# Optimization experiments

Measured on AMD Instinct MI355X. Metric: run time of the kernel, lower is better.

## Reference

```python
import jax, jax.numpy as jnp
import numpy as np

EPS = 1e-8  # matches F.cosine_similarity eps clamp

def _cosine_gram(x):
    # row-normalize with eps clamp, then Gram matrix == pairwise cosine similarity
    norms = jnp.maximum(jnp.linalg.norm(x, axis=-1, keepdims=True), EPS)
    xn = x / norms
    return xn @ xn.T  # [N, N]

def setup_inputs() -> dict:
    key = jax.random.key(0)
    k1, k2 = jax.random.split(key)
    N, D = 4096, 512
    return {
        "cosine_distance_latent": jax.random.normal(k1, (N, D), dtype=jnp.float32),
        "mse_latent": jax.random.normal(k2, (N, D), dtype=jnp.float32),
    }

def reference(cosine_distance_latent, mse_latent):
    # cosine distance matrices: (sim - 1) * -1 == 1 - sim
    cd = 1.0 - _cosine_gram(cosine_distance_latent)  # target
    ed = 1.0 - _cosine_gram(mse_latent)              # predicted
    # KL(softmax(cd) || softmax(ed)) per row, then mean
    log_t = jax.nn.log_softmax(cd, axis=-1)
    log_p = jax.nn.log_softmax(ed, axis=-1)
    t = jnp.exp(log_t)
    kl = jnp.sum(t * (log_t - log_p), axis=-1)
    return jnp.mean(kl)
```

## Files before the change

kernel.cpp:

```cpp
#include <hip/hip_runtime.h>
#include <math.h>

#define NROWS 4096
#define DIM   512
#define BMI   256
#define BNJ   128
#define KSTEPS (DIM / 32)
#define NSLOT (NROWS / BNJ)
#define STB   49152

typedef __bf16 bf16x8 __attribute__((ext_vector_type(8)));
typedef float  f32x4  __attribute__((ext_vector_type(4)));

#define GL16(G, L) __builtin_amdgcn_global_load_lds( \
    (const __attribute__((address_space(1))) void*)(G), \
    (__attribute__((address_space(3))) void*)(L), 16, 0, 0)

__global__ __launch_bounds__(256)
void normalize_kernel(const float* __restrict__ X, const float* __restrict__ Y,
                      __bf16* __restrict__ Xn, __bf16* __restrict__ Yn)
{
    const int wid  = threadIdx.x >> 6;
    const int lane = threadIdx.x & 63;
    const int row  = blockIdx.x * 4 + wid;
    const float* src = blockIdx.y ? Y : X;
    __bf16*      dst = blockIdx.y ? Yn : Xn;

    const float4* s4 = reinterpret_cast<const float4*>(src + (size_t)row * DIM);
    float4 v0 = s4[lane * 2 + 0];
    float4 v1 = s4[lane * 2 + 1];
    float ss = v0.x*v0.x + v0.y*v0.y + v0.z*v0.z + v0.w*v0.w
             + v1.x*v1.x + v1.y*v1.y + v1.z*v1.z + v1.w*v1.w;
    #pragma unroll
    for (int m = 1; m < 64; m <<= 1) ss += __shfl_xor(ss, m);
    const float scale = 1.0f / fmaxf(sqrtf(ss), 1e-8f);

    bf16x8 o;
    o[0] = (__bf16)(v0.x * scale); o[1] = (__bf16)(v0.y * scale);
    o[2] = (__bf16)(v0.z * scale); o[3] = (__bf16)(v0.w * scale);
    o[4] = (__bf16)(v1.x * scale); o[5] = (__bf16)(v1.y * scale);
    o[6] = (__bf16)(v1.z * scale); o[7] = (__bf16)(v1.w * scale);
    *reinterpret_cast<bf16x8*>(dst + (size_t)row * DIM + lane * 8) = o;
}

__global__ __launch_bounds__(512, 2)
void gram_kl_kernel(const __bf16* __restrict__ Xn, const __bf16* __restrict__ Yn,
                    float4* __restrict__ partials)
{
    __shared__ char lds[3 * STB];

    const int tid  = threadIdx.x;
    const int wid  = tid >> 6;
    const int lane = tid & 63;
    const int m  = wid >> 2;
    const int q  = wid & 3;
    const int iq = q & 1;
    const int jq = q >> 1;

    const int g = blockIdx.x;
    const int x = g & 7;
    const int t = g >> 3;
    const int bi = (x & 3) * 4 + (t & 3);
    const int bj = (x >> 2) * 16 + ((t >> 2) & 7) + (t >> 5) * 8;
    const int i0 = bi * BMI;
    const int j0 = bj * BNJ;

    const int xnib = (((tid & 3) ^ ((tid >> 3) & 3)) << 4);
    const size_t so_i0 = ((size_t)(i0 + (tid >> 2)) << 10) + xnib;
    const size_t so_i1 = so_i0 + ((size_t)128 << 10);
    const size_t so_j  = ((size_t)(j0 + (tid >> 2)) << 10) + xnib;
    const int wbase = wid * 1024;

    const char* bx = (const char*)Xn;
    const char* by = (const char*)Yn;

    auto STAGE = [&](int st, int ks) {
        char* base = &lds[st * STB];
        const size_t ko = (size_t)ks << 6;
        GL16(bx + so_i0 + ko, base + 0 * 8192 + wbase);
        GL16(bx + so_i1 + ko, base + 1 * 8192 + wbase);
        GL16(by + so_i0 + ko, base + 2 * 8192 + wbase);
        GL16(by + so_i1 + ko, base + 3 * 8192 + wbase);
        GL16(bx + so_j  + ko, base + 4 * 8192 + wbase);
        GL16(by + so_j  + ko, base + 5 * 8192 + wbase);
    };

    const int rdx = ((lane & 15) << 6) + ((((lane >> 4) ^ ((lane >> 1) & 3))) << 4);
    const int ibase = m * 16384 + iq * 8192;
    const int jbase = 32768 + m * 8192 + jq * 4096;

    f32x4 acc[4][8];
    #pragma unroll
    for (int fj = 0; fj < 4; ++fj)
        #pragma unroll
        for (int fi = 0; fi < 8; ++fi)
            acc[fj][fi] = f32x4{0.f, 0.f, 0.f, 0.f};

    STAGE(0, 0);
    STAGE(1, 1);

    for (int s = 0; s < KSTEPS; ++s) {
        if (s < KSTEPS - 1) asm volatile("s_waitcnt vmcnt(6)" ::: "memory");
        else                asm volatile("s_waitcnt vmcnt(0)" ::: "memory");
        __builtin_amdgcn_s_barrier();
        asm volatile("" ::: "memory");

        const char* base = &lds[(s % 3) * STB];
        bf16x8 aJ[4], bI[8];
        #pragma unroll
        for (int fj = 0; fj < 4; ++fj)
            aJ[fj] = *reinterpret_cast<const bf16x8*>(base + jbase + fj * 1024 + rdx);
        #pragma unroll
        for (int fi = 0; fi < 8; ++fi)
            bI[fi] = *reinterpret_cast<const bf16x8*>(base + ibase + fi * 1024 + rdx);

        if (s + 2 < KSTEPS) STAGE((s + 2) % 3, s + 2);

        #pragma unroll
        for (int fj = 0; fj < 4; ++fj)
            #pragma unroll
            for (int fi = 0; fi < 8; ++fi)
                acc[fj][fi] = __builtin_amdgcn_mfma_f32_16x16x32_bf16(aJ[fj], bI[fi], acc[fj][fi], 0, 0, 0);
    }

    __syncthreads();
    if (m == 1) {
        char* dst = &lds[q * 32768 + lane * 16];
        #pragma unroll
        for (int fj = 0; fj < 4; ++fj)
            #pragma unroll
            for (int fi = 0; fi < 8; ++fi)
                *reinterpret_cast<f32x4*>(dst + (fj * 8 + fi) * 1024) = acc[fj][fi];
    }
    __syncthreads();

    float4 res[8];
    if (m == 0) {
        const char* src = &lds[q * 32768 + lane * 16];
        #pragma unroll
        for (int fi = 0; fi < 8; ++fi) {
            float S = 0.f, U = 0.f, V = 0.f, Q = 0.f;
            #pragma unroll
            for (int fj = 0; fj < 4; ++fj) {
                const f32x4 pb = *reinterpret_cast<const f32x4*>(src + (fj * 8 + fi) * 1024);
                #pragma unroll
                for (int r = 0; r < 4; ++r) {
                    const float a = -acc[fj][fi][r];
                    const float b = -pb[r];
                    const float ea = __expf(a);
                    const float eb = __expf(b);
                    S += ea; U += ea * a; V += ea * b; Q += eb;
                }
            }
            #pragma unroll
            for (int mm = 16; mm <= 32; mm <<= 1) {
                S += __shfl_xor(S, mm);
                U += __shfl_xor(U, mm);
                V += __shfl_xor(V, mm);
                Q += __shfl_xor(Q, mm);
            }
            res[fi] = float4{S, U, V, Q};
        }
        if (jq == 1 && lane < 16) {
            float4* scr = reinterpret_cast<float4*>(&lds[131072]);
            #pragma unroll
            for (int fi = 0; fi < 8; ++fi)
                scr[(iq * 8 + fi) * 16 + lane] = res[fi];
        }
    }
    __syncthreads();
    if (m == 0 && jq == 0 && lane < 16) {
        const float4* scr = reinterpret_cast<const float4*>(&lds[131072]);
        #pragma unroll
        for (int fi = 0; fi < 8; ++fi) {
            const float4 o = scr[(iq * 8 + fi) * 16 + lane];
            const int row = i0 + iq * 128 + fi * 16 + lane;
            partials[(size_t)row * NSLOT + bj] =
                float4{res[fi].x + o.x, res[fi].y + o.y, res[fi].z + o.z, res[fi].w + o.w};
        }
    }
}

__global__ __launch_bounds__(256)
void merge_kernel(const float4* __restrict__ partials, float* __restrict__ blocksum)
{
    __shared__ float w[4];
    const int row = blockIdx.x * 256 + threadIdx.x;
    float S = 0.f, U = 0.f, V = 0.f, Q = 0.f;
    #pragma unroll
    for (int s = 0; s < NSLOT; ++s) {
        const float4 p = partials[(size_t)row * NSLOT + s];
        S += p.x; U += p.y; V += p.z; Q += p.w;
    }
    float kl = (U - V) / S - logf(S) + logf(Q);
    #pragma unroll
    for (int mm = 1; mm < 64; mm <<= 1) kl += __shfl_xor(kl, mm);
    if ((threadIdx.x & 63) == 0) w[threadIdx.x >> 6] = kl;
    __syncthreads();
    if (threadIdx.x == 0) blocksum[blockIdx.x] = w[0] + w[1] + w[2] + w[3];
}

__global__ __launch_bounds__(64)
void reduce_kernel(const float* __restrict__ blocksum, float* __restrict__ out)
{
    float v = (threadIdx.x < 16) ? blocksum[threadIdx.x] : 0.f;
    #pragma unroll
    for (int mm = 1; mm < 16; mm <<= 1) v += __shfl_xor(v, mm);
    if (threadIdx.x == 0) out[0] = v / (float)NROWS;
}

extern "C" void kernel_launch(void* const* d_in, const int* in_sizes, int n_in,
                              void* d_out, int out_size, void* d_ws, size_t ws_size,
                              hipStream_t stream)
{
    const float* X = (const float*)d_in[0];
    const float* Y = (const float*)d_in[1];
    float* out = (float*)d_out;

    char* ws = (char*)d_ws;
    const size_t mat_bytes = (size_t)NROWS * DIM * sizeof(__bf16);
    __bf16* Xn = (__bf16*)ws;
    __bf16* Yn = (__bf16*)(ws + mat_bytes);
    float4* partials = (float4*)(ws + 2 * mat_bytes);
    float* blocksum = (float*)(ws + 2 * mat_bytes + (size_t)NROWS * NSLOT * sizeof(float4));

    normalize_kernel<<<dim3(NROWS / 4, 2), 256, 0, stream>>>(X, Y, Xn, Yn);
    gram_kl_kernel<<<(NROWS / BMI) * (NROWS / BNJ), 512, 0, stream>>>(Xn, Yn, partials);
    merge_kernel<<<NROWS / 256, 256, 0, stream>>>(partials, blocksum);
    reduce_kernel<<<1, 64, 0, stream>>>(blocksum, out);
}
```

Measured before the change: 60.09 us.

## Split GEMM k-step into two phases with sched barriers and MFMA priority

Each k-step of the Gram MFMA loop is split into two half-phases. Half of the I-operand LDS reads are issued, then the global prefetch, and the rest of the I-operand reads overlap with the first 16 MFMAs. Sched barriers fix the instruction order, extra workgroup barriers keep waves in step, and s_setprio raises wave priority during MFMA bursts so waves interleave memory and matrix work. The two extra barriers per k-step add synchronisation cost and may reduce the slack between waves.

```diff
diff --git a/kernel.cpp b/kernel.cpp
--- a/kernel.cpp
+++ b/kernel.cpp
@@ -15,6 +15,8 @@
 #define GL16(G, L) __builtin_amdgcn_global_load_lds( \
     (const __attribute__((address_space(1))) void*)(G), \
     (__attribute__((address_space(3))) void*)(L), 16, 0, 0)
+
+#define SB0() __builtin_amdgcn_sched_barrier(0)
 
 __global__ __launch_bounds__(256)
 void normalize_kernel(const float* __restrict__ X, const float* __restrict__ Y,
@@ -103,24 +105,50 @@
         if (s < KSTEPS - 1) asm volatile("s_waitcnt vmcnt(6)" ::: "memory");
         else                asm volatile("s_waitcnt vmcnt(0)" ::: "memory");
         __builtin_amdgcn_s_barrier();
-        asm volatile("" ::: "memory");
+        SB0();
 
         const char* base = &lds[(s % 3) * STB];
-        bf16x8 aJ[4], bI[8];
+
+        bf16x8 aJ[4], bI0[4], bI1[4];
         #pragma unroll
         for (int fj = 0; fj < 4; ++fj)
             aJ[fj] = *reinterpret_cast<const bf16x8*>(base + jbase + fj * 1024 + rdx);
         #pragma unroll
-        for (int fi = 0; fi < 8; ++fi)
-            bI[fi] = *reinterpret_cast<const bf16x8*>(base + ibase + fi * 1024 + rdx);
-
+        for (int fi = 0; fi < 4; ++fi)
+            bI0[fi] = *reinterpret_cast<const bf16x8*>(base + ibase + fi * 1024 + rdx);
         if (s + 2 < KSTEPS) STAGE((s + 2) % 3, s + 2);
-
-        #pragma unroll
-        for (int fj = 0; fj < 4; ++fj)
-            #pragma unroll
-            for (int fi = 0; fi < 8; ++fi)
-                acc[fj][fi] = __builtin_amdgcn_mfma_f32_16x16x32_bf16(aJ[fj], bI[fi], acc[fj][fi], 0, 0, 0);
+        SB0();
+
+        __builtin_amdgcn_s_barrier();
+        asm volatile("s_waitcnt lgkmcnt(0)" ::: "memory");
+        SB0();
+
+        #pragma unroll
+        for (int fi = 0; fi < 4; ++fi)
+            bI1[fi] = *reinterpret_cast<const bf16x8*>(base + ibase + (4 + fi) * 1024 + rdx);
+        SB0();
+
+        __builtin_amdgcn_s_setprio(1);
+        #pragma unroll
+        for (int fj = 0; fj < 4; ++fj)
+            #pragma unroll
+            for (int fi = 0; fi < 4; ++fi)
+                acc[fj][fi] = __builtin_amdgcn_mfma_f32_16x16x32_bf16(aJ[fj], bI0[fi], acc[fj][fi], 0, 0, 0);
+        __builtin_amdgcn_s_setprio(0);
+        SB0();
+
+        __builtin_amdgcn_s_barrier();
+        asm volatile("s_waitcnt lgkmcnt(0)" ::: "memory");
+        SB0();
+
+        __builtin_amdgcn_s_setprio(1);
+        #pragma unroll
+        for (int fj = 0; fj < 4; ++fj)
+            #pragma unroll
+            for (int fi = 0; fi < 4; ++fi)
+                acc[fj][4 + fi] = __builtin_amdgcn_mfma_f32_16x16x32_bf16(aJ[fj], bI1[fi], acc[fj][4 + fi], 0, 0, 0);
+        __builtin_amdgcn_s_setprio(0);
+        SB0();
     }
 
     __syncthreads();
```

Measured after the change: 64.78 us. 7.8% more time.

## Exploit Gram matrix symmetry by computing only lower-triangular tiles

Applied to the files above, without the earlier changes.

The two Gram matrices are symmetric, so the kernel now computes only the lower-triangular 128x128 tiles. Each off-diagonal tile produces per-row softmax partial sums for both its row block and its transposed column block, written to separate partial slots. This roughly halves the MFMA work and the operand loads. In exchange, tiles shrink to 128x128 with 256 threads, the pipeline drops from triple to double buffering with a full vmcnt(0) wait each step, and the epilogue gains extra shuffle reductions.

```diff
diff --git a/kernel.cpp b/kernel.cpp
--- a/kernel.cpp
+++ b/kernel.cpp
@@ -3,11 +3,11 @@
 
 #define NROWS 4096
 #define DIM   512
-#define BMI   256
-#define BNJ   128
+#define UNIT  128
+#define NP    (NROWS / UNIT)
+#define NTILES (NP * (NP + 1) / 2)
 #define KSTEPS (DIM / 32)
-#define NSLOT (NROWS / BNJ)
-#define STB   49152
+#define NSLOT NP
 
 typedef __bf16 bf16x8 __attribute__((ext_vector_type(8)));
 typedef float  f32x4  __attribute__((ext_vector_type(4)));
@@ -43,140 +43,178 @@
     *reinterpret_cast<bf16x8*>(dst + (size_t)row * DIM + lane * 8) = o;
 }
 
-__global__ __launch_bounds__(512, 2)
+__global__ __launch_bounds__(256, 2)
 void gram_kl_kernel(const __bf16* __restrict__ Xn, const __bf16* __restrict__ Yn,
                     float4* __restrict__ partials)
 {
-    __shared__ char lds[3 * STB];
+    __shared__ char lds[69632];
 
     const int tid  = threadIdx.x;
     const int wid  = tid >> 6;
     const int lane = tid & 63;
-    const int m  = wid >> 2;
-    const int q  = wid & 3;
-    const int iq = q & 1;
-    const int jq = q >> 1;
-
-    const int g = blockIdx.x;
-    const int x = g & 7;
-    const int t = g >> 3;
-    const int bi = (x & 3) * 4 + (t & 3);
-    const int bj = (x >> 2) * 16 + ((t >> 2) & 7) + (t >> 5) * 8;
-    const int i0 = bi * BMI;
-    const int j0 = bj * BNJ;
+    const int m  = wid >> 1;
+    const int iq = wid & 1;
+
+    const int glin = (blockIdx.x & 7) * (NTILES / 8) + (blockIdx.x >> 3);
+    int p = (int)((sqrtf((float)(8 * glin + 1)) - 1.0f) * 0.5f);
+    while ((p + 1) * (p + 2) / 2 <= glin) ++p;
+    while (p * (p + 1) / 2 > glin) --p;
+    const int qcol = glin - p * (p + 1) / 2;
+    const int i0 = p * UNIT;
+    const int j0 = qcol * UNIT;
 
     const int xnib = (((tid & 3) ^ ((tid >> 3) & 3)) << 4);
-    const size_t so_i0 = ((size_t)(i0 + (tid >> 2)) << 10) + xnib;
-    const size_t so_i1 = so_i0 + ((size_t)128 << 10);
-    const size_t so_j  = ((size_t)(j0 + (tid >> 2)) << 10) + xnib;
+    const int r0 = tid >> 2;
+    const size_t so_i = ((size_t)(i0 + r0) << 10) + xnib;
+    const size_t so_j = ((size_t)(j0 + r0) << 10) + xnib;
     const int wbase = wid * 1024;
 
     const char* bx = (const char*)Xn;
     const char* by = (const char*)Yn;
 
     auto STAGE = [&](int st, int ks) {
-        char* base = &lds[st * STB];
+        char* base = &lds[st * 32768];
         const size_t ko = (size_t)ks << 6;
-        GL16(bx + so_i0 + ko, base + 0 * 8192 + wbase);
-        GL16(bx + so_i1 + ko, base + 1 * 8192 + wbase);
-        GL16(by + so_i0 + ko, base + 2 * 8192 + wbase);
-        GL16(by + so_i1 + ko, base + 3 * 8192 + wbase);
-        GL16(bx + so_j  + ko, base + 4 * 8192 + wbase);
-        GL16(by + so_j  + ko, base + 5 * 8192 + wbase);
+        const size_t h = (size_t)64 << 10;
+        GL16(bx + so_i + ko,     base + 0 * 8192 + wbase);
+        GL16(bx + so_i + h + ko, base + 0 * 8192 + 4096 + wbase);
+        GL16(by + so_i + ko,     base + 1 * 8192 + wbase);
+        GL16(by + so_i + h + ko, base + 1 * 8192 + 4096 + wbase);
+        GL16(bx + so_j + ko,     base + 2 * 8192 + wbase);
+        GL16(bx + so_j + h + ko, base + 2 * 8192 + 4096 + wbase);
+        GL16(by + so_j + ko,     base + 3 * 8192 + wbase);
+        GL16(by + so_j + h + ko, base + 3 * 8192 + 4096 + wbase);
     };
 
     const int rdx = ((lane & 15) << 6) + ((((lane >> 4) ^ ((lane >> 1) & 3))) << 4);
-    const int ibase = m * 16384 + iq * 8192;
-    const int jbase = 32768 + m * 8192 + jq * 4096;
-
-    f32x4 acc[4][8];
-    #pragma unroll
-    for (int fj = 0; fj < 4; ++fj)
-        #pragma unroll
-        for (int fi = 0; fi < 8; ++fi)
+    const int ibase = m * 8192 + iq * 4096;
+    const int jbase = 16384 + m * 8192;
+
+    f32x4 acc[8][4];
+    #pragma unroll
+    for (int fj = 0; fj < 8; ++fj)
+        #pragma unroll
+        for (int fi = 0; fi < 4; ++fi)
             acc[fj][fi] = f32x4{0.f, 0.f, 0.f, 0.f};
 
     STAGE(0, 0);
-    STAGE(1, 1);
 
     for (int s = 0; s < KSTEPS; ++s) {
-        if (s < KSTEPS - 1) asm volatile("s_waitcnt vmcnt(6)" ::: "memory");
-        else                asm volatile("s_waitcnt vmcnt(0)" ::: "memory");
+        asm volatile("s_waitcnt vmcnt(0)" ::: "memory");
         __builtin_amdgcn_s_barrier();
         asm volatile("" ::: "memory");
 
-        const char* base = &lds[(s % 3) * STB];
-        bf16x8 aJ[4], bI[8];
-        #pragma unroll
-        for (int fj = 0; fj < 4; ++fj)
+        const char* base = &lds[(s & 1) * 32768];
+        bf16x8 aJ[8], bI[4];
+        #pragma unroll
+        for (int fj = 0; fj < 8; ++fj)
             aJ[fj] = *reinterpret_cast<const bf16x8*>(base + jbase + fj * 1024 + rdx);
         #pragma unroll
-        for (int fi = 0; fi < 8; ++fi)
+        for (int fi = 0; fi < 4; ++fi)
             bI[fi] = *reinterpret_cast<const bf16x8*>(base + ibase + fi * 1024 + rdx);
 
-        if (s + 2 < KSTEPS) STAGE((s + 2) % 3, s + 2);
-
-        #pragma unroll
-        for (int fj = 0; fj < 4; ++fj)
-            #pragma unroll
-            for (int fi = 0; fi < 8; ++fi)
+        if (s + 1 < KSTEPS) STAGE((s + 1) & 1, s + 1);
+
+        #pragma unroll
+        for (int fj = 0; fj < 8; ++fj)
+            #pragma unroll
+            for (int fi = 0; fi < 4; ++fi)
                 acc[fj][fi] = __builtin_amdgcn_mfma_f32_16x16x32_bf16(aJ[fj], bI[fi], acc[fj][fi], 0, 0, 0);
     }
 
     __syncthreads();
     if (m == 1) {
-        char* dst = &lds[q * 32768 + lane * 16];
-        #pragma unroll
-        for (int fj = 0; fj < 4; ++fj)
-            #pragma unroll
-            for (int fi = 0; fi < 8; ++fi)
-                *reinterpret_cast<f32x4*>(dst + (fj * 8 + fi) * 1024) = acc[fj][fi];
-    }
-    __syncthreads();
-
-    float4 res[8];
+        char* dst = &lds[iq * 32768 + lane * 16];
+        #pragma unroll
+        for (int fj = 0; fj < 8; ++fj)
+            #pragma unroll
+            for (int fi = 0; fi < 4; ++fi)
+                *reinterpret_cast<f32x4*>(dst + (fj * 4 + fi) * 1024) = acc[fj][fi];
+    }
+    __syncthreads();
+
+    float* jpart = reinterpret_cast<float*>(&lds[65536]);
+
     if (m == 0) {
-        const char* src = &lds[q * 32768 + lane * 16];
-        #pragma unroll
-        for (int fi = 0; fi < 8; ++fi) {
-            float S = 0.f, U = 0.f, V = 0.f, Q = 0.f;
-            #pragma unroll
-            for (int fj = 0; fj < 4; ++fj) {
-                const f32x4 pb = *reinterpret_cast<const f32x4*>(src + (fj * 8 + fi) * 1024);
+        const char* src = &lds[iq * 32768 + lane * 16];
+        const int sub = lane >> 4;
+        float Si[4] = {0,0,0,0}, Ui[4] = {0,0,0,0}, Vi[4] = {0,0,0,0}, Qi[4] = {0,0,0,0};
+
+        #pragma unroll
+        for (int fj = 0; fj < 8; ++fj) {
+            f32x4 pb[4];
+            #pragma unroll
+            for (int fi = 0; fi < 4; ++fi)
+                pb[fi] = *reinterpret_cast<const f32x4*>(src + (fj * 4 + fi) * 1024);
+
+            float js[4][4];
+            #pragma unroll
+            for (int r = 0; r < 4; ++r) { js[r][0]=0; js[r][1]=0; js[r][2]=0; js[r][3]=0; }
+
+            #pragma unroll
+            for (int fi = 0; fi < 4; ++fi)
                 #pragma unroll
                 for (int r = 0; r < 4; ++r) {
                     const float a = -acc[fj][fi][r];
-                    const float b = -pb[r];
+                    const float b = -pb[fi][r];
                     const float ea = __expf(a);
                     const float eb = __expf(b);
-                    S += ea; U += ea * a; V += ea * b; Q += eb;
+                    Si[fi] += ea; Ui[fi] += ea * a; Vi[fi] += ea * b; Qi[fi] += eb;
+                    js[r][0] += ea; js[r][1] += ea * a; js[r][2] += ea * b; js[r][3] += eb;
+                }
+
+            if (p != qcol) {
+                #pragma unroll
+                for (int r = 0; r < 4; ++r)
+                    #pragma unroll
+                    for (int qq = 0; qq < 4; ++qq) {
+                        #pragma unroll
+                        for (int mk = 1; mk <= 8; mk <<= 1)
+                            js[r][qq] += __shfl_xor(js[r][qq], mk);
+                    }
+                if ((lane & 15) == 0) {
+                    #pragma unroll
+                    for (int r = 0; r < 4; ++r)
+                        #pragma unroll
+                        for (int qq = 0; qq < 4; ++qq)
+                            jpart[(((iq * 4 + sub) * 8 + fj) * 4 + r) * 4 + qq] = js[r][qq];
                 }
             }
-            #pragma unroll
-            for (int mm = 16; mm <= 32; mm <<= 1) {
-                S += __shfl_xor(S, mm);
-                U += __shfl_xor(U, mm);
-                V += __shfl_xor(V, mm);
-                Q += __shfl_xor(Q, mm);
+        }
+
+        #pragma unroll
+        for (int fi = 0; fi < 4; ++fi) {
+            #pragma unroll
+            for (int mk = 16; mk <= 32; mk <<= 1) {
+                Si[fi] += __shfl_xor(Si[fi], mk);
+                Ui[fi] += __shfl_xor(Ui[fi], mk);
+                Vi[fi] += __shfl_xor(Vi[fi], mk);
+                Qi[fi] += __shfl_xor(Qi[fi], mk);
             }
-            res[fi] = float4{S, U, V, Q};
-        }
-        if (jq == 1 && lane < 16) {
-            float4* scr = reinterpret_cast<float4*>(&lds[131072]);
-            #pragma unroll
-            for (int fi = 0; fi < 8; ++fi)
-                scr[(iq * 8 + fi) * 16 + lane] = res[fi];
-        }
-    }
-    __syncthreads();
-    if (m == 0 && jq == 0 && lane < 16) {
-        const float4* scr = reinterpret_cast<const float4*>(&lds[131072]);
-        #pragma unroll
-        for (int fi = 0; fi < 8; ++fi) {
-            const float4 o = scr[(iq * 8 + fi) * 16 + lane];
-            const int row = i0 + iq * 128 + fi * 16 + lane;
-            partials[(size_t)row * NSLOT + bj] =
-                float4{res[fi].x + o.x, res[fi].y + o.y, res[fi].z + o.z, res[fi].w + o.w};
+        }
+        if (lane < 16) {
+            #pragma unroll
+            for (int fi = 0; fi < 4; ++fi) {
+                const int row = i0 + iq * 64 + fi * 16 + lane;
+                partials[(size_t)row * NSLOT + qcol] = float4{Si[fi], Ui[fi], Vi[fi], Qi[fi]};
+            }
+        }
+    }
+    __syncthreads();
+
+    if (p != qcol && wid == 0) {
+        #pragma unroll
+        for (int h = 0; h < 2; ++h) {
+            const int j = h * 64 + lane;
+            const int fj = j >> 4, sub = (j >> 2) & 3, r = j & 3;
+            const int o0 = (((0 * 4 + sub) * 8 + fj) * 4 + r) * 4;
+            const int o1 = (((1 * 4 + sub) * 8 + fj) * 4 + r) * 4;
+            float4 v;
+            v.x = jpart[o0 + 0] + jpart[o1 + 0];
+            v.y = jpart[o0 + 1] + jpart[o1 + 1];
+            v.z = jpart[o0 + 2] + jpart[o1 + 2];
+            v.w = jpart[o0 + 3] + jpart[o1 + 3];
+            partials[(size_t)(j0 + j) * NSLOT + p] = v;
         }
     }
 }
@@ -225,7 +263,7 @@
     float* blocksum = (float*)(ws + 2 * mat_bytes + (size_t)NROWS * NSLOT * sizeof(float4));
 
     normalize_kernel<<<dim3(NROWS / 4, 2), 256, 0, stream>>>(X, Y, Xn, Yn);
-    gram_kl_kernel<<<(NROWS / BMI) * (NROWS / BNJ), 512, 0, stream>>>(Xn, Yn, partials);
+    gram_kl_kernel<<<NTILES, 256, 0, stream>>>(Xn, Yn, partials);
     merge_kernel<<<NROWS / 256, 256, 0, stream>>>(partials, blocksum);
     reduce_kernel<<<1, 64, 0, stream>>>(blocksum, out);
 }
```

After: 156.5 us. 2.6x slower.
